# Kernel tuning notes

Measured on AMD Instinct MI355X. Metric: run time of the kernel, lower is better.

Reference implementation:

```python
import jax, jax.numpy as jnp
import numpy as np

N_TETS = 200000
IN_FEATURES = 128
OUT_FEATURES = 128
NUM_NEIGHBORS = 4  # NEIGHBORHOOD_SIZE = 5 = self + 4 neighbors


def setup_inputs() -> dict:
    key = jax.random.key(0)
    k1, k2, k3, k4 = jax.random.split(key, 4)
    features = jax.random.normal(k1, (N_TETS, IN_FEATURES), dtype=jnp.float32)
    neighbors = jax.random.randint(k2, (N_TETS, NUM_NEIGHBORS), 0, N_TETS, dtype=jnp.int64)
    # torch nn.Linear convention: W is [out_features, 5*in_features]
    fan_in = (1 + NUM_NEIGHBORS) * IN_FEATURES
    bound = 1.0 / np.sqrt(fan_in)
    W = jax.random.uniform(k3, (OUT_FEATURES, fan_in), minval=-bound, maxval=bound, dtype=jnp.float32)
    b = jax.random.uniform(k4, (OUT_FEATURES,), minval=-bound, maxval=bound, dtype=jnp.float32)
    return {"features": features, "neighbors": neighbors, "W": W, "b": b}


def reference(features, neighbors, W, b):
    # Gather neighbor features: [N, 4, F]
    nbr_feats = features[neighbors]
    N = features.shape[0]
    # Concat self + 4 neighbors along feature dim -> [N, 5F]
    stacked = jnp.concatenate([features[:, None, :], nbr_feats], axis=1).reshape(N, -1)
    # Linear + ReLU (torch: x @ W.T + b)
    return jax.nn.relu(stacked @ W.T + b)
```

## Files before the change

kernel.cpp:

```cpp
#include <hip/hip_runtime.h>
#include <stdint.h>

#define NTETS   200000
#define FEATS   128
#define OUTF    128
#define NG      5
#define BM      128
#define NTHR    512
#define NBLOCKS ((NTETS + BM - 1) / BM)

typedef __attribute__((ext_vector_type(8))) short  short8v;
typedef __attribute__((ext_vector_type(4))) float  f32x4;

static __device__ __forceinline__ unsigned short bf16_rne(float f) {
  union { float f; unsigned u; } v; v.f = f;
  unsigned r = v.u + 0x7FFFu + ((v.u >> 16) & 1u);
  return (unsigned short)(r >> 16);
}

static __device__ __forceinline__ void gload_lds16(const void* g, void* l) {
  __builtin_amdgcn_global_load_lds(
      (const __attribute__((address_space(1))) unsigned int*)g,
      (__attribute__((address_space(3))) unsigned int*)l, 16, 0, 0);
}

__global__ void detect_mode_k(const int* __restrict__ nbr, int* __restrict__ flag) {
  int t = threadIdx.x;
  int nz = 0;
  for (int i = t; i < 4096; i += 64) nz |= nbr[2 * i + 1];
  unsigned long long any = __ballot(nz != 0);
  if (t == 0) flag[0] = (any == 0ULL) ? 1 : 0;
}

__global__ void prep_wfrag_k(const float* __restrict__ W, unsigned short* __restrict__ wf) {
  int id = blockIdx.x * 256 + threadIdx.x;
  if (id >= NG * 16384) return;
  int e  = id & 7;
  int lk = (id >> 3) & 3;
  int lr = (id >> 5) & 15;
  int ns = (id >> 9) & 1;
  int wn = (id >> 10) & 3;
  int kk = (id >> 12) & 3;
  int g  = id >> 14;
  int n = wn * 32 + ns * 16 + lr;
  int k = g * 128 + kk * 32 + lk * 8 + e;
  wf[id] = bf16_rne(W[n * (NG * FEATS) + k]);
}

__global__ __launch_bounds__(256) void prep_f_k(const float* __restrict__ feat,
                                                unsigned short* __restrict__ fimg) {
  size_t i = ((size_t)blockIdx.x * 256 + threadIdx.x) * 8;
  f32x4 a = *(const f32x4*)(feat + i);
  f32x4 b = *(const f32x4*)(feat + i + 4);
  short8v v;
  v[0] = (short)bf16_rne(a[0]); v[1] = (short)bf16_rne(a[1]);
  v[2] = (short)bf16_rne(a[2]); v[3] = (short)bf16_rne(a[3]);
  v[4] = (short)bf16_rne(b[0]); v[5] = (short)bf16_rne(b[1]);
  v[6] = (short)bf16_rne(b[2]); v[7] = (short)bf16_rne(b[3]);
  *(short8v*)(fimg + i) = v;
}

__global__ __launch_bounds__(NTHR, 4) void conv_k(
    const unsigned short* __restrict__ fimg, const int* __restrict__ nbr,
    const float* __restrict__ bias, const unsigned short* __restrict__ wf,
    const int* __restrict__ mode, float* __restrict__ out)
{
  __shared__ __align__(16) char atile[2][32768];
  __shared__ unsigned srcoff[NG][BM];

  const int t    = threadIdx.x;
  const int row0 = blockIdx.x * BM;
  const int lane = t & 63;
  const int wv   = t >> 6;
  const int wm   = wv >> 2;
  const int wn   = wv & 3;
  const int lr   = lane & 15;
  const int lk   = lane >> 4;

  {
    const bool m64 = (mode[0] != 0);
    for (int e = t; e < NG * BM; e += NTHR) {
      int g = e >> 7, r = e & (BM - 1);
      int gr = row0 + r;
      int s = 0;
      if (gr < NTETS) {
        if (g == 0) s = gr;
        else {
          size_t idx = (size_t)gr * 4 + (g - 1);
          s = m64 ? nbr[2 * idx] : nbr[idx];
          if ((unsigned)s >= (unsigned)NTETS) s = 0;
        }
      }
      srcoff[g][r] = (unsigned)s * 256u;
    }
  }
  __syncthreads();

  const int arow_lo = lane >> 4;
  const unsigned apos = (unsigned)((lane & 15) << 4);

#define ISSUE_A(g_, buf_) do {                                                  \
    _Pragma("unroll")                                                           \
    for (int i_ = 0; i_ < 4; ++i_) {                                            \
      int r_ = wv * 16 + i_ * 4 + arow_lo;                                      \
      unsigned o_ = srcoff[g_][r_] + (apos ^ (unsigned)((r_ & 7) << 4));        \
      gload_lds16((const char*)fimg + o_, &atile[buf_][wv * 4096 + i_ * 1024]); \
    }                                                                           \
  } while (0)

  ISSUE_A(0, 0);
  ISSUE_A(1, 1);
  asm volatile("s_waitcnt vmcnt(4)" ::: "memory");
  __builtin_amdgcn_sched_barrier(0);
  __builtin_amdgcn_s_barrier();

  const f32x4 zero = {0.f, 0.f, 0.f, 0.f};
  f32x4 acc[4][2];
#pragma unroll
  for (int i = 0; i < 4; ++i) { acc[i][0] = zero; acc[i][1] = zero; }

  const int rswz  = (lr & 7) << 4;
  const int abase = (wm * 64 + lr) * 256;
  const char* wfl = (const char*)wf + (size_t)(wn * 2) * 1024 + lr * 64 + lk * 16;

#define LOADA(dst_, kk_) do {                                                   \
    _Pragma("unroll")                                                           \
    for (int ms_ = 0; ms_ < 4; ++ms_)                                           \
      dst_[ms_] = *(const short8v*)(&atile[bi][abase + ms_ * 4096 +             \
                                    ((((kk_) << 6) + (lk << 4)) ^ rswz)]);      \
  } while (0)

#define FMA8(aset_, kk_) do {                                                   \
    _Pragma("unroll")                                                           \
    for (int ms_ = 0; ms_ < 4; ++ms_)                                           \
      _Pragma("unroll")                                                         \
      for (int ns_ = 0; ns_ < 2; ++ns_)                                         \
        acc[ms_][ns_] = __builtin_amdgcn_mfma_f32_16x16x32_bf16(                \
            aset_[ms_], b[kk_][ns_], acc[ms_][ns_], 0, 0, 0);                   \
  } while (0)

#pragma unroll
  for (int g = 0; g < NG; ++g) {
    const int bi = g & 1;
    short8v b[4][2];
#pragma unroll
    for (int kk = 0; kk < 4; ++kk)
#pragma unroll
      for (int ns = 0; ns < 2; ++ns)
        b[kk][ns] = *(const short8v*)(wfl + (size_t)((g * 4 + kk) * 8 + ns) * 1024);
    __builtin_amdgcn_sched_barrier(0);

    short8v a0[4], a1[4];
    LOADA(a0, 0);
    LOADA(a1, 1);
    FMA8(a0, 0);
    LOADA(a0, 2);
    FMA8(a1, 1);
    LOADA(a1, 3);
    FMA8(a0, 2);
    if (g + 2 < NG) {
      asm volatile("s_waitcnt lgkmcnt(0)" ::: "memory");
      __builtin_amdgcn_sched_barrier(0);
      __builtin_amdgcn_s_barrier();
      ISSUE_A(g + 2, bi);
    }
    FMA8(a1, 3);
    if (g + 1 < NG) {
      if (g + 2 < NG) asm volatile("s_waitcnt vmcnt(4)" ::: "memory");
      else            asm volatile("s_waitcnt vmcnt(0)" ::: "memory");
      __builtin_amdgcn_sched_barrier(0);
      __builtin_amdgcn_s_barrier();
    }
  }

#pragma unroll
  for (int ns = 0; ns < 2; ++ns) {
    const int col = wn * 32 + ns * 16 + lr;
    const float bv = bias[col];
#pragma unroll
    for (int ms = 0; ms < 4; ++ms) {
      const int rbase = row0 + wm * 64 + ms * 16 + lk * 4;
#pragma unroll
      for (int i = 0; i < 4; ++i) {
        int r = rbase + i;
        if (r < NTETS) {
          float vv = acc[ms][ns][i] + bv;
          out[(size_t)r * OUTF + col] = vv > 0.f ? vv : 0.f;
        }
      }
    }
  }
#undef ISSUE_A
#undef LOADA
#undef FMA8
}

extern "C" void kernel_launch(void* const* d_in, const int* in_sizes, int n_in,
                              void* d_out, int out_size, void* d_ws, size_t ws_size,
                              hipStream_t stream) {
  const float* feat = (const float*)d_in[0];
  const int*   nbr  = (const int*)d_in[1];
  const float* W    = (const float*)d_in[2];
  const float* bias = (const float*)d_in[3];
  float* out = (float*)d_out;

  int* mode = (int*)d_ws;
  unsigned short* wf   = (unsigned short*)((char*)d_ws + 1024);
  unsigned short* fimg = (unsigned short*)((char*)d_ws + 164864);

  detect_mode_k<<<1, 64, 0, stream>>>(nbr, mode);
  prep_wfrag_k<<<320, 256, 0, stream>>>(W, wf);
  prep_f_k<<<(NTETS * FEATS / 8 + 255) / 256, 256, 0, stream>>>(feat, fimg);
  conv_k<<<NBLOCKS, NTHR, 0, stream>>>(fimg, nbr, bias, wf, mode, out);
}
```

Before: 128.1 us.

## Replace direct global-to-LDS loads with register-staged gather double buffering

Drops the global_load_lds direct-to-LDS path with its two-stage prefetch and manual vmcnt waits. Each group's gathered feature rows are now loaded into registers during the previous group's MFMA loop, then written to the alternate swizzled LDS buffer before a __syncthreads. The aim is simpler synchronisation and letting the compiler schedule the loads. In exchange it uses more VGPRs for the staged rows, prefetches only one group ahead instead of two, and adds LDS write instructions.

```diff
diff --git a/kernel.cpp b/kernel.cpp
--- a/kernel.cpp
+++ b/kernel.cpp
@@ -16,12 +16,6 @@
   union { float f; unsigned u; } v; v.f = f;
   unsigned r = v.u + 0x7FFFu + ((v.u >> 16) & 1u);
   return (unsigned short)(r >> 16);
-}
-
-static __device__ __forceinline__ void gload_lds16(const void* g, void* l) {
-  __builtin_amdgcn_global_load_lds(
-      (const __attribute__((address_space(1))) unsigned int*)g,
-      (__attribute__((address_space(3))) unsigned int*)l, 16, 0, 0);
 }
 
 __global__ void detect_mode_k(const int* __restrict__ nbr, int* __restrict__ flag) {
@@ -96,23 +90,8 @@
   }
   __syncthreads();
 
-  const int arow_lo = lane >> 4;
+  const int arow      = wv * 16 + (lane >> 4);
   const unsigned apos = (unsigned)((lane & 15) << 4);
-
-#define ISSUE_A(g_, buf_) do {                                                  \
-    _Pragma("unroll")                                                           \
-    for (int i_ = 0; i_ < 4; ++i_) {                                            \
-      int r_ = wv * 16 + i_ * 4 + arow_lo;                                      \
-      unsigned o_ = srcoff[g_][r_] + (apos ^ (unsigned)((r_ & 7) << 4));        \
-      gload_lds16((const char*)fimg + o_, &atile[buf_][wv * 4096 + i_ * 1024]); \
-    }                                                                           \
-  } while (0)
-
-  ISSUE_A(0, 0);
-  ISSUE_A(1, 1);
-  asm volatile("s_waitcnt vmcnt(4)" ::: "memory");
-  __builtin_amdgcn_sched_barrier(0);
-  __builtin_amdgcn_s_barrier();
 
   const f32x4 zero = {0.f, 0.f, 0.f, 0.f};
   f32x4 acc[4][2];
@@ -123,53 +102,64 @@
   const int abase = (wm * 64 + lr) * 256;
   const char* wfl = (const char*)wf + (size_t)(wn * 2) * 1024 + lr * 64 + lk * 16;
 
-#define LOADA(dst_, kk_) do {                                                   \
-    _Pragma("unroll")                                                           \
-    for (int ms_ = 0; ms_ < 4; ++ms_)                                           \
-      dst_[ms_] = *(const short8v*)(&atile[bi][abase + ms_ * 4096 +             \
-                                    ((((kk_) << 6) + (lk << 4)) ^ rswz)]);      \
+  short8v stA[4];
+  short8v b[4][2];
+
+#define GATHER_A(g_) do {                                                        \
+    _Pragma("unroll")                                                            \
+    for (int i_ = 0; i_ < 4; ++i_) {                                             \
+      int r_ = arow + i_ * 4;                                                    \
+      stA[i_] = *(const short8v*)((const char*)fimg + srcoff[g_][r_] + apos);    \
+    }                                                                            \
   } while (0)
 
-#define FMA8(aset_, kk_) do {                                                   \
-    _Pragma("unroll")                                                           \
-    for (int ms_ = 0; ms_ < 4; ++ms_)                                           \
-      _Pragma("unroll")                                                         \
-      for (int ns_ = 0; ns_ < 2; ++ns_)                                         \
-        acc[ms_][ns_] = __builtin_amdgcn_mfma_f32_16x16x32_bf16(                \
-            aset_[ms_], b[kk_][ns_], acc[ms_][ns_], 0, 0, 0);                   \
+#define WRITE_A(buf_) do {                                                       \
+    _Pragma("unroll")                                                            \
+    for (int i_ = 0; i_ < 4; ++i_) {                                             \
+      int r_ = arow + i_ * 4;                                                    \
+      *(short8v*)(&atile[buf_][r_ * 256 + (apos ^ (unsigned)((r_ & 7) << 4))]) = \
+          stA[i_];                                                               \
+    }                                                                            \
   } while (0)
+
+#define FMA8(aset_, kk_) do {                                                    \
+    _Pragma("unroll")                                                            \
+    for (int ms_ = 0; ms_ < 4; ++ms_)                                            \
+      _Pragma("unroll")                                                          \
+      for (int ns_ = 0; ns_ < 2; ++ns_)                                          \
+        acc[ms_][ns_] = __builtin_amdgcn_mfma_f32_16x16x32_bf16(                 \
+            aset_[ms_], b[kk_][ns_], acc[ms_][ns_], 0, 0, 0);                    \
+  } while (0)
+
+  GATHER_A(0);
+  WRITE_A(0);
+  __syncthreads();
 
 #pragma unroll
   for (int g = 0; g < NG; ++g) {
     const int bi = g & 1;
-    short8v b[4][2];
 #pragma unroll
     for (int kk = 0; kk < 4; ++kk)
 #pragma unroll
       for (int ns = 0; ns < 2; ++ns)
         b[kk][ns] = *(const short8v*)(wfl + (size_t)((g * 4 + kk) * 8 + ns) * 1024);
+    if (g + 1 < NG) GATHER_A(g + 1);
     __builtin_amdgcn_sched_barrier(0);
 
-    short8v a0[4], a1[4];
-    LOADA(a0, 0);
-    LOADA(a1, 1);
-    FMA8(a0, 0);
-    LOADA(a0, 2);
-    FMA8(a1, 1);
-    LOADA(a1, 3);
-    FMA8(a0, 2);
-    if (g + 2 < NG) {
-      asm volatile("s_waitcnt lgkmcnt(0)" ::: "memory");
-      __builtin_amdgcn_sched_barrier(0);
-      __builtin_amdgcn_s_barrier();
-      ISSUE_A(g + 2, bi);
-    }
-    FMA8(a1, 3);
+#pragma unroll
+    for (int kk = 0; kk < 4; ++kk) {
+      short8v a[4];
+#pragma unroll
+      for (int ms = 0; ms < 4; ++ms)
+        a[ms] = *(const short8v*)(&atile[bi][abase + ms * 4096 +
+                                  ((((kk) << 6) + (lk << 4)) ^ rswz)]);
+      FMA8(a, kk);
+    }
+    __builtin_amdgcn_sched_barrier(0);
+
     if (g + 1 < NG) {
-      if (g + 2 < NG) asm volatile("s_waitcnt vmcnt(4)" ::: "memory");
-      else            asm volatile("s_waitcnt vmcnt(0)" ::: "memory");
-      __builtin_amdgcn_sched_barrier(0);
-      __builtin_amdgcn_s_barrier();
+      WRITE_A(bi ^ 1);
+      __syncthreads();
     }
   }
 
@@ -190,8 +180,8 @@
       }
     }
   }
-#undef ISSUE_A
-#undef LOADA
+#undef GATHER_A
+#undef WRITE_A
 #undef FMA8
 }
 
```

Measured after the change: 116.3 us. -9.2%, faster.

## Stream weights through LDS and load gathered activations directly into registers

Applied to the files above, without the earlier changes.

Reverses the conv kernel's data flow. Each wave now owns 16 rows across all 128 output columns and loads its gathered bf16 feature fragments from global memory straight into registers. The weight fragments for each group are staged into double-buffered LDS with global_load_lds and shared by all 8 waves. The weight fragment prep kernel is relaid out to match. This removes the per-wave global reads of the B fragments and the LDS round-trip for the gathered A rows. In exchange, each wave does 8 B-fragment LDS reads per k-step, and the vmcnt accounting now mixes the register A loads with the LDS weight loads.

```diff
diff --git a/kernel.cpp b/kernel.cpp
--- a/kernel.cpp
+++ b/kernel.cpp
@@ -36,14 +36,12 @@
   int id = blockIdx.x * 256 + threadIdx.x;
   if (id >= NG * 16384) return;
   int e  = id & 7;
-  int lk = (id >> 3) & 3;
-  int lr = (id >> 5) & 15;
-  int ns = (id >> 9) & 1;
-  int wn = (id >> 10) & 3;
+  int l6 = (id >> 3) & 63;
+  int ns = (id >> 9) & 7;
   int kk = (id >> 12) & 3;
   int g  = id >> 14;
-  int n = wn * 32 + ns * 16 + lr;
-  int k = g * 128 + kk * 32 + lk * 8 + e;
+  int n = ns * 16 + (l6 & 15);
+  int k = g * 128 + kk * 32 + (l6 >> 4) * 8 + e;
   wf[id] = bf16_rne(W[n * (NG * FEATS) + k]);
 }
 
@@ -65,15 +63,13 @@
     const float* __restrict__ bias, const unsigned short* __restrict__ wf,
     const int* __restrict__ mode, float* __restrict__ out)
 {
-  __shared__ __align__(16) char atile[2][32768];
+  __shared__ __align__(16) char wtile[2][32768];
   __shared__ unsigned srcoff[NG][BM];
 
   const int t    = threadIdx.x;
   const int row0 = blockIdx.x * BM;
   const int lane = t & 63;
   const int wv   = t >> 6;
-  const int wm   = wv >> 2;
-  const int wn   = wv & 3;
   const int lr   = lane & 15;
   const int lk   = lane >> 4;
 
@@ -96,103 +92,92 @@
   }
   __syncthreads();
 
-  const int arow_lo = lane >> 4;
-  const unsigned apos = (unsigned)((lane & 15) << 4);
-
-#define ISSUE_A(g_, buf_) do {                                                  \
+  const char* fimgc = (const char*)fimg;
+  unsigned aoff[NG];
+#pragma unroll
+  for (int g = 0; g < NG; ++g)
+    aoff[g] = srcoff[g][wv * 16 + lr] + (unsigned)(lk * 16);
+
+  const f32x4 zero = {0.f, 0.f, 0.f, 0.f};
+  f32x4 acc[8];
+#pragma unroll
+  for (int i = 0; i < 8; ++i) acc[i] = zero;
+
+  short8v a[2][4];
+
+#define SB() __builtin_amdgcn_sched_barrier(0)
+
+#define A_ISSUE(gg) do {                                                        \
     _Pragma("unroll")                                                           \
-    for (int i_ = 0; i_ < 4; ++i_) {                                            \
-      int r_ = wv * 16 + i_ * 4 + arow_lo;                                      \
-      unsigned o_ = srcoff[g_][r_] + (apos ^ (unsigned)((r_ & 7) << 4));        \
-      gload_lds16((const char*)fimg + o_, &atile[buf_][wv * 4096 + i_ * 1024]); \
-    }                                                                           \
+    for (int kk_ = 0; kk_ < 4; ++kk_)                                           \
+      a[(gg) & 1][kk_] = *(const short8v*)(fimgc + aoff[gg] + kk_ * 64);        \
   } while (0)
 
-  ISSUE_A(0, 0);
-  ISSUE_A(1, 1);
+#define W_ISSUE(gg) do {                                                        \
+    const char* ws_ = (const char*)wf + (gg) * 32768 + wv * 4096 + (lane << 4); \
+    _Pragma("unroll")                                                           \
+    for (int i_ = 0; i_ < 4; ++i_)                                              \
+      gload_lds16(ws_ + i_ * 1024, &wtile[(gg) & 1][wv * 4096 + i_ * 1024]);    \
+  } while (0)
+
+  A_ISSUE(0); SB();
+  W_ISSUE(0); SB();
+  W_ISSUE(1); SB();
   asm volatile("s_waitcnt vmcnt(4)" ::: "memory");
-  __builtin_amdgcn_sched_barrier(0);
+  SB();
   __builtin_amdgcn_s_barrier();
-
-  const f32x4 zero = {0.f, 0.f, 0.f, 0.f};
-  f32x4 acc[4][2];
-#pragma unroll
-  for (int i = 0; i < 4; ++i) { acc[i][0] = zero; acc[i][1] = zero; }
-
-  const int rswz  = (lr & 7) << 4;
-  const int abase = (wm * 64 + lr) * 256;
-  const char* wfl = (const char*)wf + (size_t)(wn * 2) * 1024 + lr * 64 + lk * 16;
-
-#define LOADA(dst_, kk_) do {                                                   \
-    _Pragma("unroll")                                                           \
-    for (int ms_ = 0; ms_ < 4; ++ms_)                                           \
-      dst_[ms_] = *(const short8v*)(&atile[bi][abase + ms_ * 4096 +             \
-                                    ((((kk_) << 6) + (lk << 4)) ^ rswz)]);      \
-  } while (0)
-
-#define FMA8(aset_, kk_) do {                                                   \
-    _Pragma("unroll")                                                           \
-    for (int ms_ = 0; ms_ < 4; ++ms_)                                           \
-      _Pragma("unroll")                                                         \
-      for (int ns_ = 0; ns_ < 2; ++ns_)                                         \
-        acc[ms_][ns_] = __builtin_amdgcn_mfma_f32_16x16x32_bf16(                \
-            aset_[ms_], b[kk_][ns_], acc[ms_][ns_], 0, 0, 0);                   \
-  } while (0)
 
 #pragma unroll
   for (int g = 0; g < NG; ++g) {
     const int bi = g & 1;
-    short8v b[4][2];
-#pragma unroll
-    for (int kk = 0; kk < 4; ++kk)
-#pragma unroll
-      for (int ns = 0; ns < 2; ++ns)
-        b[kk][ns] = *(const short8v*)(wfl + (size_t)((g * 4 + kk) * 8 + ns) * 1024);
-    __builtin_amdgcn_sched_barrier(0);
-
-    short8v a0[4], a1[4];
-    LOADA(a0, 0);
-    LOADA(a1, 1);
-    FMA8(a0, 0);
-    LOADA(a0, 2);
-    FMA8(a1, 1);
-    LOADA(a1, 3);
-    FMA8(a0, 2);
-    if (g + 2 < NG) {
-      asm volatile("s_waitcnt lgkmcnt(0)" ::: "memory");
-      __builtin_amdgcn_sched_barrier(0);
+    if (g + 1 < NG) { A_ISSUE(g + 1); }
+    SB();
+#pragma unroll
+    for (int kk = 0; kk < 4; ++kk) {
+      short8v b[8];
+#pragma unroll
+      for (int ns = 0; ns < 8; ++ns)
+        b[ns] = *(const short8v*)(&wtile[bi][(kk * 8 + ns) * 1024 + (lane << 4)]);
+      if (kk == 3 && g + 2 < NG) {
+        asm volatile("s_waitcnt lgkmcnt(0)" ::: "memory");
+        SB();
+        __builtin_amdgcn_s_barrier();
+        W_ISSUE(g + 2);
+        SB();
+      }
+#pragma unroll
+      for (int ns = 0; ns < 8; ++ns)
+        acc[ns] = __builtin_amdgcn_mfma_f32_16x16x32_bf16(a[bi][kk], b[ns], acc[ns], 0, 0, 0);
+    }
+    SB();
+    if (g <= 2) {
+      asm volatile("s_waitcnt vmcnt(8)" ::: "memory");
+      SB();
       __builtin_amdgcn_s_barrier();
-      ISSUE_A(g + 2, bi);
-    }
-    FMA8(a1, 3);
-    if (g + 1 < NG) {
-      if (g + 2 < NG) asm volatile("s_waitcnt vmcnt(4)" ::: "memory");
-      else            asm volatile("s_waitcnt vmcnt(0)" ::: "memory");
-      __builtin_amdgcn_sched_barrier(0);
+    } else if (g == 3) {
+      asm volatile("s_waitcnt vmcnt(4)" ::: "memory");
+      SB();
       __builtin_amdgcn_s_barrier();
     }
   }
 
 #pragma unroll
-  for (int ns = 0; ns < 2; ++ns) {
-    const int col = wn * 32 + ns * 16 + lr;
+  for (int ns = 0; ns < 8; ++ns) {
+    const int col = ns * 16 + lr;
     const float bv = bias[col];
-#pragma unroll
-    for (int ms = 0; ms < 4; ++ms) {
-      const int rbase = row0 + wm * 64 + ms * 16 + lk * 4;
-#pragma unroll
-      for (int i = 0; i < 4; ++i) {
-        int r = rbase + i;
-        if (r < NTETS) {
-          float vv = acc[ms][ns][i] + bv;
-          out[(size_t)r * OUTF + col] = vv > 0.f ? vv : 0.f;
-        }
+    const int rbase = row0 + wv * 16 + lk * 4;
+#pragma unroll
+    for (int i = 0; i < 4; ++i) {
+      int r = rbase + i;
+      if (r < NTETS) {
+        float vv = acc[ns][i] + bv;
+        out[(size_t)r * OUTF + col] = vv > 0.f ? vv : 0.f;
       }
     }
   }
-#undef ISSUE_A
-#undef LOADA
-#undef FMA8
+#undef A_ISSUE
+#undef W_ISSUE
+#undef SB
 }
 
 extern "C" void kernel_launch(void* const* d_in, const int* in_sizes, int n_in,
```

Result: faster. 116.7 us (-8.9%).
